# Performance work log

Hardware: AMD Instinct MI355X
Metric: run time of the kernel (lower is better)

Reference implementation:

```python
import jax, jax.numpy as jnp
import numpy as np

RES = 16; NC = 256; NCP = 1024; KNN = 32; SIGMA = 0.1
DM = 256; NH = 8; FF = 1024; NLAYERS = 2
E = NC * 8 * (RES // 8) ** 2
EH = 8
B = 4; N = 65536


def setup_inputs() -> dict:
    key = jax.random.key(0)
    ks = jax.random.split(key, 16)
    s = 0.02
    def w(k, shape):
        return jax.random.normal(k, shape, jnp.float32) * s
    inp = {}
    inp['pc'] = jax.random.normal(ks[0], (B, N, 3), jnp.float32)
    inp['pe_w1'] = w(ks[1], (3, 128)); inp['pe_b1'] = jnp.zeros((128,), jnp.float32)
    inp['pe_w2'] = w(ks[2], (128, 128)); inp['pe_b2'] = jnp.zeros((128,), jnp.float32)
    inp['t_qkv_w'] = w(ks[3], (NLAYERS, DM, 3 * DM)); inp['t_qkv_b'] = jnp.zeros((NLAYERS, 3 * DM), jnp.float32)
    inp['t_out_w'] = w(ks[4], (NLAYERS, DM, DM)); inp['t_out_b'] = jnp.zeros((NLAYERS, DM), jnp.float32)
    inp['t_ln1_s'] = jnp.ones((NLAYERS, DM), jnp.float32); inp['t_ln1_b'] = jnp.zeros((NLAYERS, DM), jnp.float32)
    inp['t_ff1_w'] = w(ks[5], (NLAYERS, DM, FF)); inp['t_ff1_b'] = jnp.zeros((NLAYERS, FF), jnp.float32)
    inp['t_ff2_w'] = w(ks[6], (NLAYERS, FF, DM)); inp['t_ff2_b'] = jnp.zeros((NLAYERS, DM), jnp.float32)
    inp['t_ln2_s'] = jnp.ones((NLAYERS, DM), jnp.float32); inp['t_ln2_b'] = jnp.zeros((NLAYERS, DM), jnp.float32)
    inp['c1_w'] = w(ks[7], (2 * NC, NC, 3, 3)); inp['c1_b'] = jnp.zeros((2 * NC,), jnp.float32)
    inp['c2_w'] = w(ks[8], (4 * NC, 2 * NC, 3, 3)); inp['c2_b'] = jnp.zeros((4 * NC,), jnp.float32)
    inp['c3_w'] = w(ks[9], (8 * NC, 4 * NC, 3, 3)); inp['c3_b'] = jnp.zeros((8 * NC,), jnp.float32)
    inp['x_qkv_w'] = w(ks[10], (E, 3 * E)); inp['x_qkv_b'] = jnp.zeros((3 * E,), jnp.float32)
    inp['x_out_w'] = w(ks[11], (E, E)); inp['x_out_b'] = jnp.zeros((E,), jnp.float32)
    return inp


def _layernorm(x, s, b):
    m = x.mean(-1, keepdims=True)
    v = ((x - m) ** 2).mean(-1, keepdims=True)
    return (x - m) / jnp.sqrt(v + 1e-5) * s + b


def _mha(x, qkv_w, qkv_b, out_w, out_b, nh):
    Bq, S, D = x.shape
    dh = D // nh
    qkv = x @ qkv_w + qkv_b
    q, k, v = jnp.split(qkv, 3, axis=-1)
    def sp(t):
        return t.reshape(Bq, S, nh, dh).transpose(0, 2, 1, 3)
    q, k, v = sp(q), sp(k), sp(v)
    a = jax.nn.softmax(jnp.einsum('bhqd,bhkd->bhqk', q, k) / jnp.sqrt(jnp.float32(dh)), axis=-1)
    o = jnp.einsum('bhqk,bhkd->bhqd', a, v).transpose(0, 2, 1, 3).reshape(Bq, S, D)
    return o @ out_w + out_b


def _density(pc):
    # faithful to source: distance to the FIRST k points (unsorted), not kNN
    d = jnp.linalg.norm(pc[:, :, None, :] - pc[:, None, :KNN, :], axis=-1)  # (B,N,k)
    return jnp.exp(-2.0 * SIGMA ** 2 / (d * d + 1e-6)).mean(axis=-1)


def _fps_indices(pc, density):
    # incremental min-dist FPS: selects identical points to the original O(N*K^2) loop
    def one(pc_b, dens_b):
        first = jnp.argmax(dens_b)
        mind = jnp.linalg.norm(pc_b - pc_b[first], axis=-1)
        def step(mind, _):
            idx = jnp.argmax(mind)
            d = jnp.linalg.norm(pc_b - pc_b[idx], axis=-1)
            return jnp.minimum(mind, d), idx
        _, rest = jax.lax.scan(step, mind, None, length=NCP - 1)
        return jnp.concatenate([first[None], rest])
    return jax.vmap(one)(pc, density)


def _forward(pc, idx, pe_w1, pe_b1, pe_w2, pe_b2, t_qkv_w, t_qkv_b, t_out_w, t_out_b,
             t_ln1_s, t_ln1_b, t_ff1_w, t_ff1_b, t_ff2_w, t_ff2_b, t_ln2_s, t_ln2_b,
             c1_w, c1_b, c2_w, c2_b, c3_w, c3_b, x_qkv_w, x_qkv_b, x_out_w, x_out_b):
    Bq = pc.shape[0]
    centers = jnp.take_along_axis(pc, idx[:, :, None], axis=1)  # (B,K,3)
    # point encoder MLP -> (B,K,128)
    f = jax.nn.relu(centers @ pe_w1 + pe_b1) @ pe_w2 + pe_b2
    # sinusoidal pos-emb per axis, mean over xyz -> (B,K,128)
    half = 64
    freqs = jnp.exp(jnp.arange(half, dtype=jnp.float32) * (-np.log(10000.0) / (half - 1)))
    e = centers[..., None] * freqs  # (B,K,3,64)
    pos = jnp.concatenate([jnp.sin(e), jnp.cos(e)], axis=-1).mean(axis=2)
    x = jnp.concatenate([f, pos], axis=-1)  # (B,K,256)
    # 2-layer post-LN transformer encoder
    for l in range(NLAYERS):
        h = _mha(x, t_qkv_w[l], t_qkv_b[l], t_out_w[l], t_out_b[l], NH)
        x = _layernorm(x + h, t_ln1_s[l], t_ln1_b[l])
        h = jax.nn.relu(x @ t_ff1_w[l] + t_ff1_b[l]) @ t_ff2_w[l] + t_ff2_b[l]
        x = _layernorm(x + h, t_ln2_s[l], t_ln2_b[l])
    # scatter-add features onto three planes
    L = pc.max() - pc.min()
    def grid(c):
        return jnp.clip(((c + L / 2) / L * RES).astype(jnp.int32), 0, RES - 1)
    gx = grid(centers[..., 0]); gy = grid(centers[..., 1]); gz = grid(centers[..., 2])
    tri = jnp.zeros((Bq, 3, RES, RES, DM), jnp.float32)  # channels last for scatter
    bi = jnp.arange(Bq)[:, None]
    tri = tri.at[bi, 0, gy, gx].add(x)
    tri = tri.at[bi, 1, gz, gy].add(x)
    tri = tri.at[bi, 2, gz, gx].add(x)
    tri = tri.transpose(0, 1, 4, 2, 3)  # (B,3,C,R,R)
    z = tri.reshape(Bq * 3, DM, RES, RES)
    def conv(xx, w, b):
        y = jax.lax.conv_general_dilated(xx, w, (2, 2), ((1, 1), (1, 1)),
                                         dimension_numbers=('NCHW', 'OIHW', 'NCHW'))
        return y + b[None, :, None, None]
    z = jax.nn.relu(conv(z, c1_w, c1_b))
    z = jax.nn.relu(conv(z, c2_w, c2_b))
    z = jax.nn.relu(conv(z, c3_w, c3_b))  # (B*3, 8C, R/8, R/8)
    flat = z.reshape(Bq, 3, E)
    attn = _mha(flat, x_qkv_w, x_qkv_b, x_out_w, x_out_b, EH)
    return attn.reshape(Bq, 3, 8 * NC, RES // 8, RES // 8)


def reference(pc, pe_w1, pe_b1, pe_w2, pe_b2, t_qkv_w, t_qkv_b, t_out_w, t_out_b,
              t_ln1_s, t_ln1_b, t_ff1_w, t_ff1_b, t_ff2_w, t_ff2_b, t_ln2_s, t_ln2_b,
              c1_w, c1_b, c2_w, c2_b, c3_w, c3_b, x_qkv_w, x_qkv_b, x_out_w, x_out_b):
    idx = _fps_indices(pc, _density(pc))
    return _forward(pc, idx, pe_w1, pe_b1, pe_w2, pe_b2, t_qkv_w, t_qkv_b, t_out_w, t_out_b,
                    t_ln1_s, t_ln1_b, t_ff1_w, t_ff1_b, t_ff2_w, t_ff2_b, t_ln2_s, t_ln2_b,
                    c1_w, c1_b, c2_w, c2_b, c3_w, c3_b, x_qkv_w, x_qkv_b, x_out_w, x_out_b)
```

## Files before the change

### kernel.cpp

```cpp
#include <hip/hip_runtime.h>
#include <math.h>

#define NPTS   65536
#define NBATCH 4
#define KCP    1024
#define DM     256
#define FFD    1024
#define EDIM   8192
#define N3E    24576

#define FPS_NBLK 16
#define FPS_THR  256
#define FPS_PPT  16
#define GPUB     8
#define HARV_MAX 16
#define RING     16
#define TSPLIT   512

typedef __attribute__((ext_vector_type(8))) short short8v;
typedef __attribute__((ext_vector_type(4))) short short4v;
typedef __attribute__((ext_vector_type(4))) float float4v;

__device__ __forceinline__ unsigned long long umaxll(unsigned long long a, unsigned long long b) {
  return a > b ? a : b;
}

__device__ __forceinline__ short bf16rn(float f) {
  unsigned u = __float_as_uint(f);
  return (short)((u + 0x7FFFu + ((u >> 16) & 1u)) >> 16);
}

__global__ __launch_bounds__(256) void redmm_kernel(const float* __restrict__ v, int n,
                                                    float* __restrict__ pmax, float* __restrict__ pmin) {
  float mx = -INFINITY, mn = INFINITY;
  for (int i = blockIdx.x * 256 + threadIdx.x; i < n; i += gridDim.x * 256) {
    float x = v[i]; mx = fmaxf(mx, x); mn = fminf(mn, x);
  }
#pragma unroll
  for (int off = 32; off >= 1; off >>= 1) {
    mx = fmaxf(mx, __shfl_xor(mx, off, 64));
    mn = fminf(mn, __shfl_xor(mn, off, 64));
  }
  __shared__ float smx[4], smn[4];
  int lane = threadIdx.x & 63, w = threadIdx.x >> 6;
  if (lane == 0) { smx[w] = mx; smn[w] = mn; }
  __syncthreads();
  if (threadIdx.x == 0) {
    pmax[blockIdx.x] = fmaxf(fmaxf(smx[0], smx[1]), fmaxf(smx[2], smx[3]));
    pmin[blockIdx.x] = fminf(fminf(smn[0], smn[1]), fminf(smn[2], smn[3]));
  }
}

__global__ __launch_bounds__(256) void redfin_kernel(const float* __restrict__ pmax,
                                                     const float* __restrict__ pmin, int nb,
                                                     float* __restrict__ Lv) {
  float mx = -INFINITY, mn = INFINITY;
  for (int i = threadIdx.x; i < nb; i += 256) { mx = fmaxf(mx, pmax[i]); mn = fminf(mn, pmin[i]); }
#pragma unroll
  for (int off = 32; off >= 1; off >>= 1) {
    mx = fmaxf(mx, __shfl_xor(mx, off, 64));
    mn = fminf(mn, __shfl_xor(mn, off, 64));
  }
  __shared__ float smx[4], smn[4];
  int lane = threadIdx.x & 63, w = threadIdx.x >> 6;
  if (lane == 0) { smx[w] = mx; smn[w] = mn; }
  __syncthreads();
  if (threadIdx.x == 0) {
    mx = fmaxf(fmaxf(smx[0], smx[1]), fmaxf(smx[2], smx[3]));
    mn = fminf(fminf(smn[0], smn[1]), fminf(smn[2], smn[3]));
    Lv[0] = __fsub_rn(mx, mn);
  }
}

__global__ __launch_bounds__(FPS_THR, 1) void fps_kernel(const float* __restrict__ pc,
                                                         float* __restrict__ centers,
                                                         unsigned* __restrict__ tags,
                                                         unsigned long long* __restrict__ keys,
                                                         float* __restrict__ mindbuf,
                                                         int* __restrict__ state,
                                                         int phase) {
  const int blk = blockIdx.x;
  const int b = blk / FPS_NBLK, bb = blk % FPS_NBLK;
  const int tid = threadIdx.x;
  const int lane = tid & 63, wv = tid >> 6;
  const int wvg = bb * 4 + wv;
  const float* pcb = pc + (size_t)b * NPTS * 3;

  __shared__ float kpts[96];
  __shared__ float wlds[2][HARV_MAX][3];
  __shared__ int hcnt[2];

  float px[FPS_PPT], py[FPS_PPT], pz[FPS_PPT], mind[FPS_PPT];
  const int gbase = wvg * 1024;
#pragma unroll
  for (int i = 0; i < FPS_PPT; ++i) {
    int g = gbase + i * 64 + lane;
    px[i] = pcb[3 * g]; py[i] = pcb[3 * g + 1]; pz[i] = pcb[3 * g + 2];
  }

  unsigned* const tagb = tags + (size_t)b * RING * 64;
  unsigned long long* const keyb = keys + (size_t)b * RING * 64 * GPUB;
  float* const mb = mindbuf + ((size_t)b * 64 + wvg) * FPS_PPT * 64;

  int t, r;
  if (phase == 0) {
    for (int i = tid; i < 96; i += FPS_THR) kpts[i] = pcb[i];
    __syncthreads();
    unsigned long long bk = 0ull;
#pragma unroll
    for (int i = 0; i < FPS_PPT; ++i) {
      float acc = 0.f;
      for (int j = 0; j < 32; ++j) {
        float dx = __fsub_rn(px[i], kpts[3 * j]);
        float dy = __fsub_rn(py[i], kpts[3 * j + 1]);
        float dz = __fsub_rn(pz[i], kpts[3 * j + 2]);
        float ss = __fadd_rn(__fadd_rn(__fmul_rn(dx, dx), __fmul_rn(dy, dy)), __fmul_rn(dz, dz));
        float d = __fsqrt_rn(ss);
        float dd = __fadd_rn(__fmul_rn(d, d), 1e-6f);
        acc = __fadd_rn(acc, expf(__fdiv_rn(-0.02f, dd)));
      }
      float dens = __fdiv_rn(acc, 32.f);
      int g = gbase + i * 64 + lane;
      bk = umaxll(bk, ((unsigned long long)__float_as_uint(dens) << 32) | (unsigned int)(~g));
    }
#pragma unroll
    for (int off = 1; off < 64; off <<= 1) bk = umaxll(bk, __shfl_xor(bk, off, 64));
    if (lane == 0) {
      keyb[(size_t)(1 & (RING - 1)) * 64 * GPUB + wvg * GPUB] = bk;
      __hip_atomic_store(&tagb[(1 & (RING - 1)) * 64 + wvg], 1u, __ATOMIC_RELEASE, __HIP_MEMORY_SCOPE_AGENT);
    }
    unsigned tag;
    do {
      tag = __hip_atomic_load(&tagb[(1 & (RING - 1)) * 64 + lane], __ATOMIC_ACQUIRE, __HIP_MEMORY_SCOPE_AGENT);
    } while (__any(tag != 1u));
    unsigned long long k2 = __hip_atomic_load(&keyb[(size_t)(1 & (RING - 1)) * 64 * GPUB + lane * GPUB],
                                              __ATOMIC_RELAXED, __HIP_MEMORY_SCOPE_AGENT);
#pragma unroll
    for (int off = 1; off < 64; off <<= 1) k2 = umaxll(k2, __shfl_xor(k2, off, 64));
    int widx = (int)(~(unsigned)(k2 & 0xFFFFFFFFull));
    float wx = pcb[3 * widx], wy = pcb[3 * widx + 1], wz = pcb[3 * widx + 2];
    if (wvg == 0 && lane == 0) {
      centers[(size_t)b * KCP * 3 + 0] = wx;
      centers[(size_t)b * KCP * 3 + 1] = wy;
      centers[(size_t)b * KCP * 3 + 2] = wz;
    }
#pragma unroll
    for (int i = 0; i < FPS_PPT; ++i) {
      float dx = __fsub_rn(px[i], wx), dy = __fsub_rn(py[i], wy), dz = __fsub_rn(pz[i], wz);
      mind[i] = __fsqrt_rn(__fadd_rn(__fadd_rn(__fmul_rn(dx, dx), __fmul_rn(dy, dy)), __fmul_rn(dz, dz)));
    }
    t = 1; r = 2;
  } else {
    r = state[b * 2]; t = state[b * 2 + 1];
#pragma unroll
    for (int i = 0; i < FPS_PPT; ++i) mind[i] = mb[i * 64 + lane];
  }

  const int tend = phase ? KCP : TSPLIT;
  while (t < tend) {
    unsigned long long tk[FPS_PPT];
#pragma unroll
    for (int i = 0; i < FPS_PPT; ++i) {
      int g = gbase + i * 64 + lane;
      tk[i] = ((unsigned long long)__float_as_uint(mind[i]) << 32) | (unsigned int)(~g);
    }
    unsigned long long ek[GPUB];
#pragma unroll
    for (int g = 0; g < GPUB; ++g) {
      unsigned long long lbk = 0ull;
#pragma unroll
      for (int i = 0; i < FPS_PPT; ++i) lbk = umaxll(lbk, tk[i]);
      unsigned long long wk = lbk;
#pragma unroll
      for (int off = 1; off < 64; off <<= 1) wk = umaxll(wk, __shfl_xor(wk, off, 64));
      ek[g] = wk;
#pragma unroll
      for (int i = 0; i < FPS_PPT; ++i)
        if (tk[i] == wk) tk[i] = 0ull;
    }
    const int ri = r & (RING - 1);
    if (lane == 0) {
      unsigned long long* sp = keyb + ((size_t)ri * 64 + wvg) * GPUB;
#pragma unroll
      for (int g = 0; g < GPUB; ++g)
        __hip_atomic_store(&sp[g], ek[g], __ATOMIC_RELAXED, __HIP_MEMORY_SCOPE_AGENT);
      __hip_atomic_store(&tagb[ri * 64 + wvg], (unsigned)r, __ATOMIC_RELEASE, __HIP_MEMORY_SCOPE_AGENT);
    }

    if (wv == 0) {
      unsigned tag;
      do {
        tag = __hip_atomic_load(&tagb[ri * 64 + lane], __ATOMIC_ACQUIRE, __HIP_MEMORY_SCOPE_AGENT);
      } while (__any(tag != (unsigned)r));
      const unsigned long long* pl = keyb + ((size_t)ri * 64 + lane) * GPUB;
      unsigned long long ck[GPUB];
#pragma unroll
      for (int e = 0; e < GPUB; ++e)
        ck[e] = __hip_atomic_load(&pl[e], __ATOMIC_RELAXED, __HIP_MEMORY_SCOPE_AGENT);
      float cx[GPUB], cy[GPUB], cz[GPUB];
#pragma unroll
      for (int e = 0; e < GPUB; ++e) {
        int gi = (int)(~(unsigned)(ck[e] & 0xFFFFFFFFull));
        cx[e] = pcb[3 * gi]; cy[e] = pcb[3 * gi + 1]; cz[e] = pcb[3 * gi + 2];
      }
      unsigned long long u = ck[GPUB - 1];
#pragma unroll
      for (int off = 1; off < 64; off <<= 1) u = umaxll(u, __shfl_xor(u, off, 64));
      int h = 0, tl = t;
      while (true) {
        unsigned long long lb = 0ull; float lx = 0.f, ly = 0.f, lz = 0.f;
#pragma unroll
        for (int e = 0; e < GPUB; ++e)
          if (ck[e] > lb) { lb = ck[e]; lx = cx[e]; ly = cy[e]; lz = cz[e]; }
        unsigned long long wk = lb;
#pragma unroll
        for (int off = 1; off < 64; off <<= 1) wk = umaxll(wk, __shfl_xor(wk, off, 64));
        if (h > 0 && wk < u) break;
        int owner = __ffsll(__ballot(lb == wk)) - 1;
        float wx = __shfl(lx, owner, 64), wy = __shfl(ly, owner, 64), wz = __shfl(lz, owner, 64);
        if (lane == 0) {
          wlds[r & 1][h][0] = wx; wlds[r & 1][h][1] = wy; wlds[r & 1][h][2] = wz;
          if (bb == 0) {
            centers[((size_t)b * KCP + tl) * 3 + 0] = wx;
            centers[((size_t)b * KCP + tl) * 3 + 1] = wy;
            centers[((size_t)b * KCP + tl) * 3 + 2] = wz;
          }
        }
#pragma unroll
        for (int e = 0; e < GPUB; ++e) {
          float dx = __fsub_rn(cx[e], wx), dy = __fsub_rn(cy[e], wy), dz = __fsub_rn(cz[e], wz);
          float d = __fsqrt_rn(__fadd_rn(__fadd_rn(__fmul_rn(dx, dx), __fmul_rn(dy, dy)), __fmul_rn(dz, dz)));
          float ov = __uint_as_float((unsigned)(ck[e] >> 32));
          float nv = fminf(ov, d);
          ck[e] = ((unsigned long long)__float_as_uint(nv) << 32) | (ck[e] & 0xFFFFFFFFull);
        }
        ++h; ++tl;
        if (h == HARV_MAX || tl == KCP) break;
      }
      if (lane == 0) hcnt[r & 1] = h;
    }
    __syncthreads();
    const int h = hcnt[r & 1];
    for (int j = 0; j < h; ++j) {
      float wx = wlds[r & 1][j][0], wy = wlds[r & 1][j][1], wz = wlds[r & 1][j][2];
#pragma unroll
      for (int i = 0; i < FPS_PPT; ++i) {
        float dx = __fsub_rn(px[i], wx), dy = __fsub_rn(py[i], wy), dz = __fsub_rn(pz[i], wz);
        float d = __fsqrt_rn(__fadd_rn(__fadd_rn(__fmul_rn(dx, dx), __fmul_rn(dy, dy)), __fmul_rn(dz, dz)));
        mind[i] = fminf(mind[i], d);
      }
    }
    t += h; ++r;
  }

  if (phase == 0) {
#pragma unroll
    for (int i = 0; i < FPS_PPT; ++i) mb[i * 64 + lane] = mind[i];
    if (bb == 0 && wv == 0 && lane == 0) { state[b * 2] = r; state[b * 2 + 1] = t; }
  }
}

__global__ __launch_bounds__(128) void pe_kernel(const float* __restrict__ centers,
                                                 const float* __restrict__ w1, const float* __restrict__ b1,
                                                 const float* __restrict__ w2, const float* __restrict__ b2,
                                                 float* __restrict__ x) {
  const int p = blockIdx.x;
  const int d = threadIdx.x;
  __shared__ float h[128];
  __shared__ float c[3];
  if (d < 3) c[d] = centers[(size_t)p * 3 + d];
  __syncthreads();
  float hv = b1[d];
#pragma unroll
  for (int j = 0; j < 3; ++j) hv += c[j] * w1[j * 128 + d];
  hv = fmaxf(hv, 0.f);
  h[d] = hv;
  __syncthreads();
  float f = b2[d];
  for (int j = 0; j < 128; ++j) f += h[j] * w2[j * 128 + d];
  x[(size_t)p * 256 + d] = f;
  if (d < 64) {
    float fr = expf(__fmul_rn((float)d, -0.14619587892025696f));
    float ssum = 0.f, csum = 0.f;
#pragma unroll
    for (int a = 0; a < 3; ++a) {
      float e = __fmul_rn(c[a], fr);
      ssum += sinf(e); csum += cosf(e);
    }
    x[(size_t)p * 256 + 128 + d] = __fdiv_rn(ssum, 3.f);
    x[(size_t)p * 256 + 192 + d] = __fdiv_rn(csum, 3.f);
  }
}

__global__ __launch_bounds__(256) void gemm_mfma_kernel(const float* __restrict__ A,
                                                        const float* __restrict__ W,
                                                        const float* __restrict__ bias,
                                                        float* __restrict__ C,
                                                        int M, int Kd, int Nd, int relu) {
  __shared__ __align__(16) short Al[128][40];
  __shared__ __align__(16) short Wl[128][40];
  const int bm = blockIdx.y * 128, bn = blockIdx.x * 128;
  const int tid = threadIdx.x;
  const int lane = tid & 63, wv = tid >> 6;
  const int wr = wv >> 1, wc = wv & 1;
  const int l15 = lane & 15, lk = lane >> 4;

  float4v acc[4][4];
#pragma unroll
  for (int i = 0; i < 4; ++i)
#pragma unroll
    for (int j = 0; j < 4; ++j) acc[i][j] = (float4v){0.f, 0.f, 0.f, 0.f};

  for (int k0 = 0; k0 < Kd; k0 += 32) {
    __syncthreads();
#pragma unroll
    for (int i = 0; i < 4; ++i) {
      int idx = (i * 256 + tid) * 4;
      int m = idx >> 5, k = idx & 31;
      float4 v = *(const float4*)&A[(size_t)(bm + m) * Kd + k0 + k];
      short4v s = { bf16rn(v.x), bf16rn(v.y), bf16rn(v.z), bf16rn(v.w) };
      *(short4v*)&Al[m][k] = s;
    }
#pragma unroll
    for (int i = 0; i < 4; ++i) {
      int task = i * 256 + tid;
      int n = task & 127, c = task >> 7;
      short4v s;
#pragma unroll
      for (int j = 0; j < 4; ++j)
        s[j] = bf16rn(W[(size_t)(k0 + c * 4 + j) * Nd + bn + n]);
      *(short4v*)&Wl[n][c * 4] = s;
    }
    __syncthreads();
    short8v af[4], bf[4];
#pragma unroll
    for (int mf = 0; mf < 4; ++mf)
      af[mf] = *(const short8v*)&Al[wr * 64 + mf * 16 + l15][lk * 8];
#pragma unroll
    for (int nf = 0; nf < 4; ++nf)
      bf[nf] = *(const short8v*)&Wl[wc * 64 + nf * 16 + l15][lk * 8];
#pragma unroll
    for (int mf = 0; mf < 4; ++mf)
#pragma unroll
      for (int nf = 0; nf < 4; ++nf)
        acc[mf][nf] = __builtin_amdgcn_mfma_f32_16x16x32_bf16(af[mf], bf[nf], acc[mf][nf], 0, 0, 0);
  }

#pragma unroll
  for (int mf = 0; mf < 4; ++mf) {
    int row = bm + wr * 64 + mf * 16 + lk * 4;
#pragma unroll
    for (int nf = 0; nf < 4; ++nf) {
      int col = bn + wc * 64 + nf * 16 + l15;
      float bv = bias[col];
#pragma unroll
      for (int j = 0; j < 4; ++j) {
        float v = acc[mf][nf][j] + bv;
        if (relu) v = fmaxf(v, 0.f);
        C[(size_t)(row + j) * Nd + col] = v;
      }
    }
  }
}

__global__ __launch_bounds__(256, 1) void flash_mfma_kernel(const float* __restrict__ qkv,
                                                            float* __restrict__ ao) {
  const int qt = blockIdx.x, h = blockIdx.y, b = blockIdx.z;
  const int tid = threadIdx.x;
  const int lane = tid & 63, w = tid >> 6;
  const int l15 = lane & 15, lk = lane >> 4;
  const int q0 = qt * 64;

  __shared__ __align__(16) short Kc[64][40];
  __shared__ __align__(16) short Vt[32][72];
  __shared__ __align__(16) short Plds[4][16][72];

  short8v qa;
  {
    const float* qr = qkv + (size_t)(b * 1024 + q0 + w * 16 + l15) * 768 + h * 32 + lk * 8;
    float4 a = *(const float4*)qr;
    float4 c = *(const float4*)(qr + 4);
    qa = (short8v){ bf16rn(a.x), bf16rn(a.y), bf16rn(a.z), bf16rn(a.w),
                    bf16rn(c.x), bf16rn(c.y), bf16rn(c.z), bf16rn(c.w) };
  }

  float4v o0 = (float4v){0.f, 0.f, 0.f, 0.f};
  float4v o1 = (float4v){0.f, 0.f, 0.f, 0.f};
  float m_cur[4] = { -INFINITY, -INFINITY, -INFINITY, -INFINITY };
  float l_part[4] = { 0.f, 0.f, 0.f, 0.f };
  const float scale = 0.17677669529663687f;

  for (int c0 = 0; c0 < 1024; c0 += 64) {
    __syncthreads();
    {
      int key = tid >> 2, dblk = (tid & 3) * 8;
      size_t row = (size_t)(b * 1024 + c0 + key) * 768 + h * 32 + dblk;
      float4 k1 = *(const float4*)&qkv[row + 256];
      float4 k2 = *(const float4*)&qkv[row + 260];
      short8v ks = (short8v){ bf16rn(k1.x), bf16rn(k1.y), bf16rn(k1.z), bf16rn(k1.w),
                              bf16rn(k2.x), bf16rn(k2.y), bf16rn(k2.z), bf16rn(k2.w) };
      *(short8v*)&Kc[key][dblk] = ks;
      float4 v1 = *(const float4*)&qkv[row + 512];
      float4 v2 = *(const float4*)&qkv[row + 516];
      Vt[dblk + 0][key] = bf16rn(v1.x); Vt[dblk + 1][key] = bf16rn(v1.y);
      Vt[dblk + 2][key] = bf16rn(v1.z); Vt[dblk + 3][key] = bf16rn(v1.w);
      Vt[dblk + 4][key] = bf16rn(v2.x); Vt[dblk + 5][key] = bf16rn(v2.y);
      Vt[dblk + 6][key] = bf16rn(v2.z); Vt[dblk + 7][key] = bf16rn(v2.w);
    }
    __syncthreads();

    float4v s[4];
#pragma unroll
    for (int f = 0; f < 4; ++f) {
      short8v kb = *(const short8v*)&Kc[f * 16 + l15][lk * 8];
      float4v z = (float4v){0.f, 0.f, 0.f, 0.f};
      s[f] = __builtin_amdgcn_mfma_f32_16x16x32_bf16(qa, kb, z, 0, 0, 0);
    }
#pragma unroll
    for (int f = 0; f < 4; ++f)
#pragma unroll
      for (int j = 0; j < 4; ++j) s[f][j] *= scale;

    float corr[4];
#pragma unroll
    for (int j = 0; j < 4; ++j) {
      float v = fmaxf(fmaxf(s[0][j], s[1][j]), fmaxf(s[2][j], s[3][j]));
#pragma unroll
      for (int off = 1; off < 16; off <<= 1) v = fmaxf(v, __shfl_xor(v, off, 64));
      float m_new = fmaxf(m_cur[j], v);
      corr[j] = expf(m_cur[j] - m_new);
      m_cur[j] = m_new;
    }
#pragma unroll
    for (int f = 0; f < 4; ++f)
#pragma unroll
      for (int j = 0; j < 4; ++j) {
        float p = expf(s[f][j] - m_cur[j]);
        s[f][j] = p;
        Plds[w][lk * 4 + j][f * 16 + l15] = bf16rn(p);
      }
#pragma unroll
    for (int j = 0; j < 4; ++j) {
      float tsum = s[0][j] + s[1][j] + s[2][j] + s[3][j];
#pragma unroll
      for (int off = 1; off < 16; off <<= 1) tsum += __shfl_xor(tsum, off, 64);
      l_part[j] = l_part[j] * corr[j] + tsum;
      o0[j] *= corr[j];
      o1[j] *= corr[j];
    }
    asm volatile("s_waitcnt lgkmcnt(0)" ::: "memory");
    __builtin_amdgcn_sched_barrier(0);

#pragma unroll
    for (int kb = 0; kb < 2; ++kb) {
      short8v pa = *(const short8v*)&Plds[w][l15][kb * 32 + lk * 8];
      short8v vb0 = *(const short8v*)&Vt[l15][kb * 32 + lk * 8];
      short8v vb1 = *(const short8v*)&Vt[16 + l15][kb * 32 + lk * 8];
      o0 = __builtin_amdgcn_mfma_f32_16x16x32_bf16(pa, vb0, o0, 0, 0, 0);
      o1 = __builtin_amdgcn_mfma_f32_16x16x32_bf16(pa, vb1, o1, 0, 0, 0);
    }
  }

#pragma unroll
  for (int j = 0; j < 4; ++j) {
    float inv = 1.f / l_part[j];
    int q = q0 + w * 16 + lk * 4 + j;
    float* orow = ao + (size_t)(b * 1024 + q) * 256 + h * 32;
    orow[l15] = o0[j] * inv;
    orow[16 + l15] = o1[j] * inv;
  }
}

__global__ __launch_bounds__(256) void ln_kernel(const float* __restrict__ a, const float* __restrict__ r,
                                                 const float* __restrict__ sc, const float* __restrict__ bi,
                                                 float* __restrict__ out) {
  const int row = blockIdx.x * 4 + (threadIdx.x >> 6);
  const int lane = threadIdx.x & 63;
  const float* ar = a + (size_t)row * 256;
  const float* rr = r + (size_t)row * 256;
  float v[4];
#pragma unroll
  for (int i = 0; i < 4; ++i) v[i] = ar[lane + 64 * i] + rr[lane + 64 * i];
  float s = v[0] + v[1] + v[2] + v[3];
#pragma unroll
  for (int off = 32; off >= 1; off >>= 1) s += __shfl_xor(s, off, 64);
  float mean = s * (1.f / 256.f);
  float vs = 0.f;
#pragma unroll
  for (int i = 0; i < 4; ++i) { float d = v[i] - mean; vs += d * d; }
#pragma unroll
  for (int off = 32; off >= 1; off >>= 1) vs += __shfl_xor(vs, off, 64);
  float var = vs * (1.f / 256.f);
  float rstd = 1.f / sqrtf(var + 1e-5f);
  float* orow = out + (size_t)row * 256;
#pragma unroll
  for (int i = 0; i < 4; ++i) {
    int d = lane + 64 * i;
    orow[d] = (v[i] - mean) * rstd * sc[d] + bi[d];
  }
}

__global__ __launch_bounds__(256) void scatter_kernel(const float* __restrict__ x,
                                                      const float* __restrict__ centers,
                                                      const float* __restrict__ Lv,
                                                      float* __restrict__ tri) {
  const int pnt = blockIdx.x;
  const int b = pnt >> 10;
  const int tid = threadIdx.x;
  __shared__ int g[3];
  if (tid == 0) {
    float L = Lv[0];
    float half = __fmul_rn(L, 0.5f);
#pragma unroll
    for (int a = 0; a < 3; ++a) {
      float c = centers[(size_t)pnt * 3 + a];
      float t = __fmul_rn(__fdiv_rn(__fadd_rn(c, half), L), 16.f);
      int gi = (int)t;
      g[a] = min(15, max(0, gi));
    }
  }
  __syncthreads();
  const int gx = g[0], gy = g[1], gz = g[2];
  float v = x[(size_t)pnt * 256 + tid];
  float* trib = tri + (size_t)b * 3 * 256 * 256;
  atomicAdd(&trib[(0 * 256 + tid) * 256 + gy * 16 + gx], v);
  atomicAdd(&trib[(1 * 256 + tid) * 256 + gz * 16 + gy], v);
  atomicAdd(&trib[(2 * 256 + tid) * 256 + gz * 16 + gx], v);
}

template <int IC, int OC, int IH, int IW, int OH, int OW, int OCT, int ICC>
__global__ __launch_bounds__(256, 1) void conv_kernel(const float* __restrict__ in, const float* __restrict__ w,
                                                      const float* __restrict__ bias, float* __restrict__ out) {
  __shared__ float lin[ICC * IH * IW];
  const int n = blockIdx.x;
  const int oc = blockIdx.y * OCT + threadIdx.x / (OH * OW);
  const int sp = threadIdx.x % (OH * OW);
  const int oy = sp / OW, ox = sp % OW;
  const int iy0 = oy * 2 - 1, ix0 = ox * 2 - 1;
  float acc = 0.f;
  for (int c0 = 0; c0 < IC; c0 += ICC) {
    __syncthreads();
    for (int i = threadIdx.x; i < ICC * IH * IW; i += 256)
      lin[i] = in[((size_t)n * IC + c0) * (IH * IW) + i];
    __syncthreads();
    const float* wp = w + ((size_t)oc * IC + c0) * 9;
    for (int ic = 0; ic < ICC; ++ic) {
      const float* wr = wp + (size_t)ic * 9;
      const float* lr = lin + ic * IH * IW;
#pragma unroll
      for (int ky = 0; ky < 3; ++ky) {
        int iy = iy0 + ky;
        if (iy >= 0 && iy < IH) {
#pragma unroll
          for (int kx = 0; kx < 3; ++kx) {
            int ix = ix0 + kx;
            if (ix >= 0 && ix < IW) acc += lr[iy * IW + ix] * wr[ky * 3 + kx];
          }
        }
      }
    }
  }
  out[((size_t)n * OC + oc) * (OH * OW) + sp] = fmaxf(acc + bias[oc], 0.f);
}

__global__ __launch_bounds__(256, 1) void conv3g_kernel(const float* __restrict__ in,
                                                        const float* __restrict__ w,
                                                        const float* __restrict__ bias,
                                                        float* __restrict__ out) {
  __shared__ float wl[9216];
  __shared__ float psum[48][4];
  const int oc = blockIdx.x;
  const int tid = threadIdx.x;
  const float4* w4 = (const float4*)(w + (size_t)oc * 9216);
  for (int i = tid; i < 2304; i += 256)
    ((float4*)wl)[i] = w4[i];
  __syncthreads();
  if (tid < 192) {
    const int o = tid % 48, c = tid / 48;
    const int n = o >> 2, sp = o & 3;
    const int oy = sp >> 1, ox = sp & 1;
    const int iy0 = oy * 2 - 1, ix0 = ox * 2 - 1;
    float acc = 0.f;
    const float* inb = in + ((size_t)n * 1024 + c * 256) * 16;
    const float* wb = wl + c * 256 * 9;
    for (int ic = 0; ic < 256; ++ic) {
      const float* lr = inb + ic * 16;
      const float* wr = wb + ic * 9;
#pragma unroll
      for (int ky = 0; ky < 3; ++ky) {
        int iy = iy0 + ky;
        if (iy >= 0 && iy < 4) {
#pragma unroll
          for (int kx = 0; kx < 3; ++kx) {
            int ix = ix0 + kx;
            if (ix >= 0 && ix < 4) acc += lr[iy * 4 + ix] * wr[ky * 3 + kx];
          }
        }
      }
    }
    psum[o][c] = acc;
  }
  __syncthreads();
  if (tid < 48) {
    float s = ((psum[tid][0] + psum[tid][1]) + psum[tid][2]) + psum[tid][3];
    int n = tid >> 2, sp = tid & 3;
    out[((size_t)n * 2048 + oc) * 4 + sp] = fmaxf(s + bias[oc], 0.f);
  }
}

template <int M, int KC>
__global__ __launch_bounds__(256, 1) void matvec_part4_kernel(const float* __restrict__ A,
                                                              const float* __restrict__ W,
                                                              float* __restrict__ part,
                                                              int Kd, int Nd) {
  __shared__ float Al[KC * M];
  const int tid = threadIdx.x;
  const int n4 = blockIdx.x * 256 + tid;
  const int nd4 = Nd >> 2;
  const int k0 = blockIdx.y * KC;
  for (int i = tid; i < KC * M; i += 256) {
    int k = i / M, m = i - k * M;
    Al[i] = A[(size_t)m * Kd + k0 + k];
  }
  __syncthreads();
  float4 acc[M];
#pragma unroll
  for (int m = 0; m < M; ++m) acc[m] = make_float4(0.f, 0.f, 0.f, 0.f);
  const float4* W4 = (const float4*)W;
  for (int k = 0; k < KC; ++k) {
    float4 wv = W4[(size_t)(k0 + k) * nd4 + n4];
#pragma unroll
    for (int m = 0; m < M; ++m) {
      float a = Al[k * M + m];
      acc[m].x += a * wv.x; acc[m].y += a * wv.y; acc[m].z += a * wv.z; acc[m].w += a * wv.w;
    }
  }
  float4* pp = (float4*)(part + ((size_t)blockIdx.y * M) * Nd);
#pragma unroll
  for (int m = 0; m < M; ++m) pp[(size_t)m * nd4 + n4] = acc[m];
}

__global__ __launch_bounds__(256) void redsum_kernel(const float* __restrict__ part,
                                                     const float* __restrict__ bias,
                                                     float* __restrict__ out, int Nd, int total) {
  int i = blockIdx.x * 256 + threadIdx.x;
  if (i < total) {
    int n = i % Nd;
    float s = bias[n];
#pragma unroll
    for (int c = 0; c < 16; ++c) s += part[(size_t)c * total + i];
    out[i] = s;
  }
}

__global__ __launch_bounds__(256) void attn3_kernel(const float* __restrict__ qkv, float* __restrict__ o) {
  const int b = blockIdx.x >> 3, h = blockIdx.x & 7;
  const float* base = qkv + (size_t)b * 3 * N3E;
  const int qo = h * 1024, ko = EDIM + h * 1024, vo = 2 * EDIM + h * 1024;
  float p[9] = {};
  for (int d = threadIdx.x; d < 1024; d += 256) {
    float q0 = base[qo + d], q1 = base[N3E + qo + d], q2 = base[2 * N3E + qo + d];
    float k0 = base[ko + d], k1 = base[N3E + ko + d], k2 = base[2 * N3E + ko + d];
    p[0] += q0 * k0; p[1] += q0 * k1; p[2] += q0 * k2;
    p[3] += q1 * k0; p[4] += q1 * k1; p[5] += q1 * k2;
    p[6] += q2 * k0; p[7] += q2 * k1; p[8] += q2 * k2;
  }
  __shared__ float red[4][9];
  __shared__ float aw[9];
  const int lane = threadIdx.x & 63, w = threadIdx.x >> 6;
#pragma unroll
  for (int e = 0; e < 9; ++e)
#pragma unroll
    for (int off = 32; off >= 1; off >>= 1) p[e] += __shfl_xor(p[e], off, 64);
  if (lane == 0)
#pragma unroll
    for (int e = 0; e < 9; ++e) red[w][e] = p[e];
  __syncthreads();
  if (threadIdx.x == 0) {
    float s[9];
#pragma unroll
    for (int e = 0; e < 9; ++e) s[e] = (red[0][e] + red[1][e] + red[2][e] + red[3][e]) / 32.f;
#pragma unroll
    for (int i = 0; i < 3; ++i) {
      float m = fmaxf(fmaxf(s[i * 3], s[i * 3 + 1]), s[i * 3 + 2]);
      float e0 = expf(s[i * 3] - m), e1 = expf(s[i * 3 + 1] - m), e2 = expf(s[i * 3 + 2] - m);
      float sm = e0 + e1 + e2;
      aw[i * 3] = e0 / sm; aw[i * 3 + 1] = e1 / sm; aw[i * 3 + 2] = e2 / sm;
    }
  }
  __syncthreads();
  for (int d = threadIdx.x; d < 1024; d += 256) {
    float v0 = base[vo + d], v1 = base[N3E + vo + d], v2 = base[2 * N3E + vo + d];
#pragma unroll
    for (int i = 0; i < 3; ++i)
      o[(size_t)(b * 3 + i) * EDIM + h * 1024 + d] = aw[i * 3] * v0 + aw[i * 3 + 1] * v1 + aw[i * 3 + 2] * v2;
  }
}

extern "C" void kernel_launch(void* const* d_in, const int* in_sizes, int n_in,
                              void* d_out, int out_size, void* d_ws, size_t ws_size,
                              hipStream_t stream) {
  const float* pc      = (const float*)d_in[0];
  const float* pe_w1   = (const float*)d_in[1];
  const float* pe_b1   = (const float*)d_in[2];
  const float* pe_w2   = (const float*)d_in[3];
  const float* pe_b2   = (const float*)d_in[4];
  const float* t_qkv_w = (const float*)d_in[5];
  const float* t_qkv_b = (const float*)d_in[6];
  const float* t_out_w = (const float*)d_in[7];
  const float* t_out_b = (const float*)d_in[8];
  const float* t_ln1_s = (const float*)d_in[9];
  const float* t_ln1_b = (const float*)d_in[10];
  const float* t_ff1_w = (const float*)d_in[11];
  const float* t_ff1_b = (const float*)d_in[12];
  const float* t_ff2_w = (const float*)d_in[13];
  const float* t_ff2_b = (const float*)d_in[14];
  const float* t_ln2_s = (const float*)d_in[15];
  const float* t_ln2_b = (const float*)d_in[16];
  const float* c1_w    = (const float*)d_in[17];
  const float* c1_b    = (const float*)d_in[18];
  const float* c2_w    = (const float*)d_in[19];
  const float* c2_b    = (const float*)d_in[20];
  const float* c3_w    = (const float*)d_in[21];
  const float* c3_b    = (const float*)d_in[22];
  const float* x_qkv_w = (const float*)d_in[23];
  const float* x_qkv_b = (const float*)d_in[24];
  const float* x_out_w = (const float*)d_in[25];
  const float* x_out_b = (const float*)d_in[26];
  float* outp = (float*)d_out;

  char* wsp = (char*)d_ws;
  auto alloc = [&](size_t bytes) { char* q = wsp; wsp += (bytes + 255) & ~(size_t)255; return q; };
  float* centers = (float*)alloc((size_t)NBATCH * KCP * 3 * 4);
  float* pmax    = (float*)alloc(512 * 4);
  float* pmin    = (float*)alloc(512 * 4);
  float* Lv      = (float*)alloc(256);
  unsigned* tags = (unsigned*)alloc((size_t)NBATCH * RING * 64 * 4);
  unsigned long long* keyss = (unsigned long long*)alloc((size_t)NBATCH * RING * 64 * GPUB * 8);
  float* mindbuf = (float*)alloc((size_t)NBATCH * NPTS * 4);
  int* fstate    = (int*)alloc(256);
  float* x  = (float*)alloc((size_t)4096 * 256 * 4);
  float* xb = (float*)alloc((size_t)4096 * 256 * 4);
  float* arena = (float*)wsp;
  float* qkvb = arena;
  float* ao   = qkvb + (size_t)4096 * 768;
  float* po   = ao + (size_t)4096 * 256;
  float* ffh  = po + (size_t)4096 * 256;
  float* ffo  = ffh + (size_t)4096 * 1024;
  float* tri  = arena;
  float* z1   = tri + (size_t)NBATCH * 3 * 256 * 256;
  float* z2   = z1 + (size_t)12 * 512 * 64;
  float* z3   = z2 + (size_t)12 * 1024 * 16;
  float* qkv2 = z3 + (size_t)12 * 8192;
  float* at2  = qkv2 + (size_t)12 * N3E;
  float* mvp  = at2 + (size_t)12 * EDIM;
  (void)in_sizes; (void)n_in; (void)out_size; (void)ws_size; (void)ffo;

  hipMemsetAsync(tags, 0, (size_t)NBATCH * RING * 64 * 4 + (size_t)NBATCH * RING * 64 * GPUB * 8, stream);

  redmm_kernel<<<512, 256, 0, stream>>>(pc, NBATCH * NPTS * 3, pmax, pmin);
  redfin_kernel<<<1, 256, 0, stream>>>(pmax, pmin, 512, Lv);

  fps_kernel<<<NBATCH * FPS_NBLK, FPS_THR, 0, stream>>>(pc, centers, tags, keyss, mindbuf, fstate, 0);
  fps_kernel<<<NBATCH * FPS_NBLK, FPS_THR, 0, stream>>>(pc, centers, tags, keyss, mindbuf, fstate, 1);

  pe_kernel<<<NBATCH * KCP, 128, 0, stream>>>(centers, pe_w1, pe_b1, pe_w2, pe_b2, x);

  for (int l = 0; l < 2; ++l) {
    gemm_mfma_kernel<<<dim3(6, 32), 256, 0, stream>>>(x, t_qkv_w + (size_t)l * 256 * 768,
                                                      t_qkv_b + (size_t)l * 768, qkvb, 4096, 256, 768, 0);
    flash_mfma_kernel<<<dim3(16, 8, 4), 256, 0, stream>>>(qkvb, ao);
    gemm_mfma_kernel<<<dim3(2, 32), 256, 0, stream>>>(ao, t_out_w + (size_t)l * 256 * 256,
                                                      t_out_b + (size_t)l * 256, po, 4096, 256, 256, 0);
    ln_kernel<<<1024, 256, 0, stream>>>(x, po, t_ln1_s + (size_t)l * 256, t_ln1_b + (size_t)l * 256, xb);
    gemm_mfma_kernel<<<dim3(8, 32), 256, 0, stream>>>(xb, t_ff1_w + (size_t)l * 256 * 1024,
                                                      t_ff1_b + (size_t)l * 1024, ffh, 4096, 256, 1024, 1);
    gemm_mfma_kernel<<<dim3(2, 32), 256, 0, stream>>>(ffh, t_ff2_w + (size_t)l * 1024 * 256,
                                                      t_ff2_b + (size_t)l * 256, ffo, 4096, 1024, 256, 0);
    ln_kernel<<<1024, 256, 0, stream>>>(xb, ffo, t_ln2_s + (size_t)l * 256, t_ln2_b + (size_t)l * 256, x);
  }

  hipMemsetAsync(tri, 0, (size_t)NBATCH * 3 * 256 * 256 * 4, stream);
  scatter_kernel<<<NBATCH * KCP, 256, 0, stream>>>(x, centers, Lv, tri);

  conv_kernel<256, 512, 16, 16, 8, 8, 4, 32><<<dim3(12, 128), 256, 0, stream>>>(tri, c1_w, c1_b, z1);
  conv_kernel<512, 1024, 8, 8, 4, 4, 16, 128><<<dim3(12, 64), 256, 0, stream>>>(z1, c2_w, c2_b, z2);
  conv3g_kernel<<<2048, 256, 0, stream>>>(z2, c3_w, c3_b, z3);

  matvec_part4_kernel<12, 512><<<dim3(N3E / 1024, 16), 256, 0, stream>>>(z3, x_qkv_w, mvp, EDIM, N3E);
  redsum_kernel<<<(12 * N3E + 255) / 256, 256, 0, stream>>>(mvp, x_qkv_b, qkv2, N3E, 12 * N3E);

  attn3_kernel<<<32, 256, 0, stream>>>(qkv2, at2);

  matvec_part4_kernel<12, 512><<<dim3(EDIM / 1024, 16), 256, 0, stream>>>(at2, x_out_w, mvp, EDIM, EDIM);
  redsum_kernel<<<(12 * EDIM + 255) / 256, 256, 0, stream>>>(mvp, x_out_b, outp, EDIM, 12 * EDIM);
}
```

Before: 4.357 ms.

## Merge two-phase FPS into one kernel; add 64-row GEMM tile for N=256 GEMMs

Runs farthest-point sampling in a single persistent launch instead of splitting it at iteration 512. This removes the spill and reload of per-point min distances and loop state through global memory, plus one launch. Separately, adds a 64x128-tile, 128-thread bf16 MFMA GEMM for the out-projection and FF2 GEMMs, doubling block count to improve CU occupancy for N=256. The smaller tile increases weight reloads per output.

```diff
diff --git a/kernel.cpp b/kernel.cpp
--- a/kernel.cpp
+++ b/kernel.cpp
@@ -15,7 +15,6 @@
 #define GPUB     8
 #define HARV_MAX 16
 #define RING     16
-#define TSPLIT   512
 
 typedef __attribute__((ext_vector_type(8))) short short8v;
 typedef __attribute__((ext_vector_type(4))) short short4v;
@@ -75,10 +74,7 @@
 __global__ __launch_bounds__(FPS_THR, 1) void fps_kernel(const float* __restrict__ pc,
                                                          float* __restrict__ centers,
                                                          unsigned* __restrict__ tags,
-                                                         unsigned long long* __restrict__ keys,
-                                                         float* __restrict__ mindbuf,
-                                                         int* __restrict__ state,
-                                                         int phase) {
+                                                         unsigned long long* __restrict__ keys) {
   const int blk = blockIdx.x;
   const int b = blk / FPS_NBLK, bb = blk % FPS_NBLK;
   const int tid = threadIdx.x;
@@ -97,15 +93,13 @@
     int g = gbase + i * 64 + lane;
     px[i] = pcb[3 * g]; py[i] = pcb[3 * g + 1]; pz[i] = pcb[3 * g + 2];
   }
+  for (int i = tid; i < 96; i += FPS_THR) kpts[i] = pcb[i];
+  __syncthreads();
 
   unsigned* const tagb = tags + (size_t)b * RING * 64;
   unsigned long long* const keyb = keys + (size_t)b * RING * 64 * GPUB;
-  float* const mb = mindbuf + ((size_t)b * 64 + wvg) * FPS_PPT * 64;
-
-  int t, r;
-  if (phase == 0) {
-    for (int i = tid; i < 96; i += FPS_THR) kpts[i] = pcb[i];
-    __syncthreads();
+
+  {
     unsigned long long bk = 0ull;
 #pragma unroll
     for (int i = 0; i < FPS_PPT; ++i) {
@@ -149,15 +143,10 @@
       float dx = __fsub_rn(px[i], wx), dy = __fsub_rn(py[i], wy), dz = __fsub_rn(pz[i], wz);
       mind[i] = __fsqrt_rn(__fadd_rn(__fadd_rn(__fmul_rn(dx, dx), __fmul_rn(dy, dy)), __fmul_rn(dz, dz)));
     }
-    t = 1; r = 2;
-  } else {
-    r = state[b * 2]; t = state[b * 2 + 1];
-#pragma unroll
-    for (int i = 0; i < FPS_PPT; ++i) mind[i] = mb[i * 64 + lane];
-  }
-
-  const int tend = phase ? KCP : TSPLIT;
-  while (t < tend) {
+  }
+
+  int t = 1;
+  for (int r = 2; t < KCP; ++r) {
     unsigned long long tk[FPS_PPT];
 #pragma unroll
     for (int i = 0; i < FPS_PPT; ++i) {
@@ -250,13 +239,7 @@
         mind[i] = fminf(mind[i], d);
       }
     }
-    t += h; ++r;
-  }
-
-  if (phase == 0) {
-#pragma unroll
-    for (int i = 0; i < FPS_PPT; ++i) mb[i * 64 + lane] = mind[i];
-    if (bb == 0 && wv == 0 && lane == 0) { state[b * 2] = r; state[b * 2 + 1] = t; }
+    t += h;
   }
 }
 
@@ -352,6 +335,76 @@
 #pragma unroll
     for (int nf = 0; nf < 4; ++nf) {
       int col = bn + wc * 64 + nf * 16 + l15;
+      float bv = bias[col];
+#pragma unroll
+      for (int j = 0; j < 4; ++j) {
+        float v = acc[mf][nf][j] + bv;
+        if (relu) v = fmaxf(v, 0.f);
+        C[(size_t)(row + j) * Nd + col] = v;
+      }
+    }
+  }
+}
+
+__global__ __launch_bounds__(128) void gemm64_mfma_kernel(const float* __restrict__ A,
+                                                          const float* __restrict__ W,
+                                                          const float* __restrict__ bias,
+                                                          float* __restrict__ C,
+                                                          int M, int Kd, int Nd, int relu) {
+  __shared__ __align__(16) short Al[64][40];
+  __shared__ __align__(16) short Wl[128][40];
+  const int bm = blockIdx.y * 64, bn = blockIdx.x * 128;
+  const int tid = threadIdx.x;
+  const int lane = tid & 63, wv = tid >> 6;
+  const int l15 = lane & 15, lk = lane >> 4;
+
+  float4v acc[4][4];
+#pragma unroll
+  for (int i = 0; i < 4; ++i)
+#pragma unroll
+    for (int j = 0; j < 4; ++j) acc[i][j] = (float4v){0.f, 0.f, 0.f, 0.f};
+
+  for (int k0 = 0; k0 < Kd; k0 += 32) {
+    __syncthreads();
+#pragma unroll
+    for (int i = 0; i < 4; ++i) {
+      int idx = (i * 128 + tid) * 4;
+      int m = idx >> 5, k = idx & 31;
+      float4 v = *(const float4*)&A[(size_t)(bm + m) * Kd + k0 + k];
+      short4v s = { bf16rn(v.x), bf16rn(v.y), bf16rn(v.z), bf16rn(v.w) };
+      *(short4v*)&Al[m][k] = s;
+    }
+#pragma unroll
+    for (int i = 0; i < 8; ++i) {
+      int task = i * 128 + tid;
+      int n = task & 127, c = task >> 7;
+      short4v s;
+#pragma unroll
+      for (int j = 0; j < 4; ++j)
+        s[j] = bf16rn(W[(size_t)(k0 + c * 4 + j) * Nd + bn + n]);
+      *(short4v*)&Wl[n][c * 4] = s;
+    }
+    __syncthreads();
+    short8v af[4], bf[4];
+#pragma unroll
+    for (int mf = 0; mf < 4; ++mf)
+      af[mf] = *(const short8v*)&Al[mf * 16 + l15][lk * 8];
+#pragma unroll
+    for (int nf = 0; nf < 4; ++nf)
+      bf[nf] = *(const short8v*)&Wl[wv * 64 + nf * 16 + l15][lk * 8];
+#pragma unroll
+    for (int mf = 0; mf < 4; ++mf)
+#pragma unroll
+      for (int nf = 0; nf < 4; ++nf)
+        acc[mf][nf] = __builtin_amdgcn_mfma_f32_16x16x32_bf16(af[mf], bf[nf], acc[mf][nf], 0, 0, 0);
+  }
+
+#pragma unroll
+  for (int mf = 0; mf < 4; ++mf) {
+    int row = bm + mf * 16 + lk * 4;
+#pragma unroll
+    for (int nf = 0; nf < 4; ++nf) {
+      int col = bn + wv * 64 + nf * 16 + l15;
       float bv = bias[col];
 #pragma unroll
       for (int j = 0; j < 4; ++j) {
@@ -737,8 +790,6 @@
   float* Lv      = (float*)alloc(256);
   unsigned* tags = (unsigned*)alloc((size_t)NBATCH * RING * 64 * 4);
   unsigned long long* keyss = (unsigned long long*)alloc((size_t)NBATCH * RING * 64 * GPUB * 8);
-  float* mindbuf = (float*)alloc((size_t)NBATCH * NPTS * 4);
-  int* fstate    = (int*)alloc(256);
   float* x  = (float*)alloc((size_t)4096 * 256 * 4);
   float* xb = (float*)alloc((size_t)4096 * 256 * 4);
   float* arena = (float*)wsp;
@@ -761,8 +812,7 @@
   redmm_kernel<<<512, 256, 0, stream>>>(pc, NBATCH * NPTS * 3, pmax, pmin);
   redfin_kernel<<<1, 256, 0, stream>>>(pmax, pmin, 512, Lv);
 
-  fps_kernel<<<NBATCH * FPS_NBLK, FPS_THR, 0, stream>>>(pc, centers, tags, keyss, mindbuf, fstate, 0);
-  fps_kernel<<<NBATCH * FPS_NBLK, FPS_THR, 0, stream>>>(pc, centers, tags, keyss, mindbuf, fstate, 1);
+  fps_kernel<<<NBATCH * FPS_NBLK, FPS_THR, 0, stream>>>(pc, centers, tags, keyss);
 
   pe_kernel<<<NBATCH * KCP, 128, 0, stream>>>(centers, pe_w1, pe_b1, pe_w2, pe_b2, x);
 
@@ -770,13 +820,13 @@
     gemm_mfma_kernel<<<dim3(6, 32), 256, 0, stream>>>(x, t_qkv_w + (size_t)l * 256 * 768,
                                                       t_qkv_b + (size_t)l * 768, qkvb, 4096, 256, 768, 0);
     flash_mfma_kernel<<<dim3(16, 8, 4), 256, 0, stream>>>(qkvb, ao);
-    gemm_mfma_kernel<<<dim3(2, 32), 256, 0, stream>>>(ao, t_out_w + (size_t)l * 256 * 256,
-                                                      t_out_b + (size_t)l * 256, po, 4096, 256, 256, 0);
+    gemm64_mfma_kernel<<<dim3(2, 64), 128, 0, stream>>>(ao, t_out_w + (size_t)l * 256 * 256,
+                                                        t_out_b + (size_t)l * 256, po, 4096, 256, 256, 0);
     ln_kernel<<<1024, 256, 0, stream>>>(x, po, t_ln1_s + (size_t)l * 256, t_ln1_b + (size_t)l * 256, xb);
     gemm_mfma_kernel<<<dim3(8, 32), 256, 0, stream>>>(xb, t_ff1_w + (size_t)l * 256 * 1024,
                                                       t_ff1_b + (size_t)l * 1024, ffh, 4096, 256, 1024, 1);
-    gemm_mfma_kernel<<<dim3(2, 32), 256, 0, stream>>>(ffh, t_ff2_w + (size_t)l * 1024 * 256,
-                                                      t_ff2_b + (size_t)l * 256, ffo, 4096, 1024, 256, 0);
+    gemm64_mfma_kernel<<<dim3(2, 64), 128, 0, stream>>>(ffh, t_ff2_w + (size_t)l * 1024 * 256,
+                                                        t_ff2_b + (size_t)l * 256, ffo, 4096, 1024, 256, 0);
     ln_kernel<<<1024, 256, 0, stream>>>(xb, ffo, t_ln2_s + (size_t)l * 256, t_ln2_b + (size_t)l * 256, x);
   }
 
```

Result: no change. 4.351 ms (-0.1%).
